# Kernel tuning notes

Measured on AMD Instinct MI355X. Metric: run time of the kernel, lower is better.

## Reference

```python
import jax, jax.numpy as jnp
import numpy as np

NUM_CLASSES = 1000
B, K = 32768, 10
EPS = 1e-7


def setup_inputs() -> dict:
    key = jax.random.key(0)
    k1, k2 = jax.random.split(key)
    outputs = jax.random.normal(k1, (B, NUM_CLASSES), dtype=jnp.float32)
    complementary_labels = jax.random.randint(k2, (B, K), 0, NUM_CLASSES, dtype=jnp.int64)
    return {"outputs": outputs, "complementary_labels": complementary_labels}


def reference(outputs, complementary_labels):
    # valid entries (label != -1); duplicates count toward num_complementary,
    # exactly as in the torch code
    valid = complementary_labels != -1                       # [B, K]
    num_complementary = valid.sum(axis=1).astype(outputs.dtype)  # [B]

    probs = jax.nn.softmax(outputs, axis=1)                  # [B, C]

    # vectorized scatter: mark complementary classes; invalid (-1) entries are
    # redirected to out-of-range index C and dropped
    b, c = outputs.shape
    rows = jnp.arange(b)[:, None]                            # [B, 1]
    safe_labels = jnp.where(valid, complementary_labels, c)  # [B, K]
    mask_comp = jnp.zeros((b, c), dtype=bool).at[rows, safe_labels].set(True, mode='drop')

    # probability mass NOT in the complementary set
    sum_non_comp = jnp.sum(probs * (~mask_comp).astype(probs.dtype), axis=1)  # [B]

    loss = -jnp.log(sum_non_comp + EPS)
    scale = (c - 1) / (c - num_complementary)
    return jnp.mean(scale * loss)
```

## Files before the change

kernel.cpp:

```cpp
#include <hip/hip_runtime.h>
#include <math.h>

#define NROWS 32768
#define NCLS  1000
#define KLBL  10
#define EPSV  1e-7f
#define WAVES_PER_BLOCK 4
#define NBLOCKS (NROWS / WAVES_PER_BLOCK)

typedef float f32x4 __attribute__((ext_vector_type(4)));

__global__ __launch_bounds__(256) void mcl_rows_kernel(
    const float* __restrict__ logits,
    const int*   __restrict__ labels,
    float*       __restrict__ partial)
{
    const int wave = threadIdx.x >> 6;
    const int lane = threadIdx.x & 63;
    const int row  = blockIdx.x * WAVES_PER_BLOCK + wave;

    const float* rowp = logits + (size_t)row * NCLS;
    const f32x4* row4 = (const f32x4*)rowp;

    int lbl = -1;
    if (lane < KLBL) lbl = labels[(size_t)row * KLBL + lane];
    const bool valid = (lbl >= 0);

    const unsigned long long bal = __ballot(valid);
    const int ncomp = __popcll(bal);

    bool dup = false;
    #pragma unroll
    for (int k = 0; k < KLBL; ++k) {
        int other = __shfl(lbl, k);
        if (k < lane && valid && other == lbl) dup = true;
    }
    const bool take = valid && !dup;
    float cval = take ? rowp[lbl] : 0.0f;

    const bool has3 = (lane < 58);
    const int  i3   = has3 ? (192 + lane) : 249;
    f32x4 v0 = row4[lane];
    f32x4 v1 = row4[64 + lane];
    f32x4 v2 = row4[128 + lane];
    f32x4 v3 = row4[i3];

    float s0 = (__expf(v0.x) + __expf(v0.y)) + (__expf(v0.z) + __expf(v0.w));
    float s1 = (__expf(v1.x) + __expf(v1.y)) + (__expf(v1.z) + __expf(v1.w));
    float s2 = (__expf(v2.x) + __expf(v2.y)) + (__expf(v2.z) + __expf(v2.w));
    float s3 = (__expf(v3.x) + __expf(v3.y)) + (__expf(v3.z) + __expf(v3.w));
    float s  = ((s0 + s1) + (s2 + (has3 ? s3 : 0.0f)));

    float c = take ? __expf(cval) : 0.0f;

    #pragma unroll
    for (int off = 32; off; off >>= 1) {
        s += __shfl_xor(s, off);
        c += __shfl_xor(c, off);
    }

    __shared__ float lds_term[WAVES_PER_BLOCK];
    if (lane == 0) {
        float sum_non_comp = (s - c) / s;
        float loss  = -logf(sum_non_comp + EPSV);
        float scale = (float)(NCLS - 1) / (float)(NCLS - ncomp);
        lds_term[wave] = scale * loss;
    }
    __syncthreads();
    if (threadIdx.x == 0) {
        partial[blockIdx.x] =
            (lds_term[0] + lds_term[1]) + (lds_term[2] + lds_term[3]);
    }
}

__global__ __launch_bounds__(1024) void mcl_reduce_kernel(
    const float* __restrict__ partial, float* __restrict__ out)
{
    __shared__ float sm[1024];
    float s = 0.0f;
    #pragma unroll
    for (int i = 0; i < NBLOCKS / 1024; ++i)
        s += partial[i * 1024 + threadIdx.x];
    sm[threadIdx.x] = s;
    __syncthreads();
    #pragma unroll
    for (int off = 512; off; off >>= 1) {
        if ((int)threadIdx.x < off) sm[threadIdx.x] += sm[threadIdx.x + off];
        __syncthreads();
    }
    if (threadIdx.x == 0) out[0] = sm[0] / (float)NROWS;
}

extern "C" void kernel_launch(void* const* d_in, const int* in_sizes, int n_in,
                              void* d_out, int out_size, void* d_ws, size_t ws_size,
                              hipStream_t stream)
{
    const float* logits = (const float*)d_in[0];
    const int*   labels = (const int*)d_in[1];
    float* partial = (float*)d_ws;
    float* out     = (float*)d_out;

    mcl_rows_kernel<<<NBLOCKS, 256, 0, stream>>>(logits, labels, partial);
    mcl_reduce_kernel<<<1, 1024, 0, stream>>>(partial, out);
}
```

Measured before the change: 27.13 us.

## Process 8 rows per wave with register double-buffered prefetch of next row

The grid shrinks from 8192 blocks of one row per wave to 1024 persistent-style blocks, where each wave handles eight consecutive rows. While it computes the current row, the wave loads the next row's logits and labels into registers, and it sums the per-row losses in a register. This is meant to hide global-load latency and cut block launch and partial-write overhead, and it also shrinks the final reduce kernel to 256 threads. The cost is more registers per thread and fewer waves in flight for latency hiding.

```diff
diff --git a/kernel.cpp b/kernel.cpp
--- a/kernel.cpp
+++ b/kernel.cpp
@@ -5,86 +5,103 @@
 #define NCLS  1000
 #define KLBL  10
 #define EPSV  1e-7f
-#define WAVES_PER_BLOCK 4
-#define NBLOCKS (NROWS / WAVES_PER_BLOCK)
+#define MAIN_BLOCKS 1024
+#define WAVES_PB 4
+#define NWAVES (MAIN_BLOCKS * WAVES_PB)
+#define ROWS_PER_WAVE (NROWS / NWAVES)
 
 typedef float f32x4 __attribute__((ext_vector_type(4)));
 
-__global__ __launch_bounds__(256) void mcl_rows_kernel(
+__global__ __launch_bounds__(256) void mcl_main_kernel(
     const float* __restrict__ logits,
     const int*   __restrict__ labels,
     float*       __restrict__ partial)
 {
-    const int wave = threadIdx.x >> 6;
-    const int lane = threadIdx.x & 63;
-    const int row  = blockIdx.x * WAVES_PER_BLOCK + wave;
-
-    const float* rowp = logits + (size_t)row * NCLS;
-    const f32x4* row4 = (const f32x4*)rowp;
-
-    int lbl = -1;
-    if (lane < KLBL) lbl = labels[(size_t)row * KLBL + lane];
-    const bool valid = (lbl >= 0);
-
-    const unsigned long long bal = __ballot(valid);
-    const int ncomp = __popcll(bal);
-
-    bool dup = false;
-    #pragma unroll
-    for (int k = 0; k < KLBL; ++k) {
-        int other = __shfl(lbl, k);
-        if (k < lane && valid && other == lbl) dup = true;
-    }
-    const bool take = valid && !dup;
-    float cval = take ? rowp[lbl] : 0.0f;
+    const int tid  = threadIdx.x;
+    const int wave = tid >> 6;
+    const int lane = tid & 63;
+    const int wg   = blockIdx.x * WAVES_PB + wave;
+    const int row0 = wg * ROWS_PER_WAVE;
 
     const bool has3 = (lane < 58);
     const int  i3   = has3 ? (192 + lane) : 249;
-    f32x4 v0 = row4[lane];
-    f32x4 v1 = row4[64 + lane];
-    f32x4 v2 = row4[128 + lane];
-    f32x4 v3 = row4[i3];
 
-    float s0 = (__expf(v0.x) + __expf(v0.y)) + (__expf(v0.z) + __expf(v0.w));
-    float s1 = (__expf(v1.x) + __expf(v1.y)) + (__expf(v1.z) + __expf(v1.w));
-    float s2 = (__expf(v2.x) + __expf(v2.y)) + (__expf(v2.z) + __expf(v2.w));
-    float s3 = (__expf(v3.x) + __expf(v3.y)) + (__expf(v3.z) + __expf(v3.w));
-    float s  = ((s0 + s1) + (s2 + (has3 ? s3 : 0.0f)));
+    const f32x4* r4 = (const f32x4*)(logits + (size_t)row0 * NCLS);
+    f32x4 a0 = r4[lane];
+    f32x4 a1 = r4[64 + lane];
+    f32x4 a2 = r4[128 + lane];
+    f32x4 a3 = r4[i3];
+    int lblA = (lane < KLBL) ? labels[(size_t)row0 * KLBL + lane] : -1;
 
-    float c = take ? __expf(cval) : 0.0f;
+    float acc = 0.0f;
 
     #pragma unroll
-    for (int off = 32; off; off >>= 1) {
-        s += __shfl_xor(s, off);
-        c += __shfl_xor(c, off);
-    }
+    for (int i = 0; i < ROWS_PER_WAVE; ++i) {
+        f32x4 b0, b1, b2, b3;
+        int lblB = -1;
+        if (i + 1 < ROWS_PER_WAVE) {
+            const f32x4* n4 = (const f32x4*)(logits + (size_t)(row0 + i + 1) * NCLS);
+            b0 = n4[lane];
+            b1 = n4[64 + lane];
+            b2 = n4[128 + lane];
+            b3 = n4[i3];
+            lblB = (lane < KLBL) ? labels[(size_t)(row0 + i + 1) * KLBL + lane] : -1;
+        }
 
-    __shared__ float lds_term[WAVES_PER_BLOCK];
-    if (lane == 0) {
+        const bool valid = (lblA >= 0);
+        const unsigned long long bal = __ballot(valid);
+        const int ncomp = __popcll(bal);
+
+        bool dup = false;
+        #pragma unroll
+        for (int k = 0; k < KLBL; ++k) {
+            int other = __shfl(lblA, k);
+            if (k < lane && valid && other == lblA) dup = true;
+        }
+        const bool take = valid && !dup;
+        const float* rowp = logits + (size_t)(row0 + i) * NCLS;
+        float cval = take ? rowp[lblA] : 0.0f;
+
+        float s0 = (__expf(a0.x) + __expf(a0.y)) + (__expf(a0.z) + __expf(a0.w));
+        float s1 = (__expf(a1.x) + __expf(a1.y)) + (__expf(a1.z) + __expf(a1.w));
+        float s2 = (__expf(a2.x) + __expf(a2.y)) + (__expf(a2.z) + __expf(a2.w));
+        float s3 = (__expf(a3.x) + __expf(a3.y)) + (__expf(a3.z) + __expf(a3.w));
+        float s  = (s0 + s1) + (s2 + (has3 ? s3 : 0.0f));
+        float c  = take ? __expf(cval) : 0.0f;
+
+        #pragma unroll
+        for (int off = 32; off; off >>= 1) {
+            s += __shfl_xor(s, off);
+            c += __shfl_xor(c, off);
+        }
+
         float sum_non_comp = (s - c) / s;
         float loss  = -logf(sum_non_comp + EPSV);
         float scale = (float)(NCLS - 1) / (float)(NCLS - ncomp);
-        lds_term[wave] = scale * loss;
+        acc += scale * loss;
+
+        a0 = b0; a1 = b1; a2 = b2; a3 = b3; lblA = lblB;
     }
+
+    __shared__ float lds_acc[WAVES_PB];
+    if (lane == 0) lds_acc[wave] = acc;
     __syncthreads();
-    if (threadIdx.x == 0) {
+    if (tid == 0) {
         partial[blockIdx.x] =
-            (lds_term[0] + lds_term[1]) + (lds_term[2] + lds_term[3]);
+            (lds_acc[0] + lds_acc[1]) + (lds_acc[2] + lds_acc[3]);
     }
 }
 
-__global__ __launch_bounds__(1024) void mcl_reduce_kernel(
+__global__ __launch_bounds__(256) void mcl_reduce_kernel(
     const float* __restrict__ partial, float* __restrict__ out)
 {
-    __shared__ float sm[1024];
-    float s = 0.0f;
-    #pragma unroll
-    for (int i = 0; i < NBLOCKS / 1024; ++i)
-        s += partial[i * 1024 + threadIdx.x];
+    __shared__ float sm[256];
+    float s = (partial[threadIdx.x]       + partial[256 + threadIdx.x]) +
+              (partial[512 + threadIdx.x] + partial[768 + threadIdx.x]);
     sm[threadIdx.x] = s;
     __syncthreads();
     #pragma unroll
-    for (int off = 512; off; off >>= 1) {
+    for (int off = 128; off; off >>= 1) {
         if ((int)threadIdx.x < off) sm[threadIdx.x] += sm[threadIdx.x + off];
         __syncthreads();
     }
@@ -100,6 +117,6 @@
     float* partial = (float*)d_ws;
     float* out     = (float*)d_out;
 
-    mcl_rows_kernel<<<NBLOCKS, 256, 0, stream>>>(logits, labels, partial);
-    mcl_reduce_kernel<<<1, 1024, 0, stream>>>(partial, out);
+    mcl_main_kernel<<<MAIN_BLOCKS, 256, 0, stream>>>(logits, labels, partial);
+    mcl_reduce_kernel<<<1, 256, 0, stream>>>(partial, out);
 }
```

After: 31.62 us. +16.5%, slower.
